# Performance work log

Measured on AMD Instinct MI355X. Metric: run time of the kernel, lower is better.

## Reference

```python
import jax, jax.numpy as jnp
import numpy as np

CLASS_EMBED_DIM = 128
TOPK = 64
EPS = float(np.finfo(float).eps)
ALPHA = 0.99


def setup_inputs() -> dict:
    key = jax.random.key(0)
    k1, k2, k3 = jax.random.split(key, 3)
    b, n, d = 16, 256, 640  # d = embed_dim + class_embed_dim
    embed_dim, inner_dim = 512, 512
    x = jax.random.normal(k1, (b, n, d), dtype=jnp.float32)
    # kaiming-normal style init: std = sqrt(2 / fan_in)
    std = (2.0 / embed_dim) ** 0.5
    Wq = jax.random.normal(k2, (embed_dim, inner_dim), dtype=jnp.float32) * std
    Wk = jax.random.normal(k3, (embed_dim, inner_dim), dtype=jnp.float32) * std
    alpha = jnp.float32(ALPHA)
    return {"x": x, "Wq": Wq, "Wk": Wk, "alpha": alpha}


def reference(x, Wq, Wk, alpha):
    b, n, d = x.shape
    xf = x.reshape(b * n, d)            # (N, embed+class)
    xe = xf[:, :-CLASS_EMBED_DIM]       # (N, embed)
    q = xe @ Wq                         # (N, inner)
    k = xe @ Wk                         # (N, inner)
    D = q.shape[1]
    # dots[i,j] = mean_d (q_i - k_j)^2, via expansion (avoids N x N x D tensor)
    q2 = jnp.sum(q * q, axis=1)
    k2 = jnp.sum(k * k, axis=1)
    dots = (q2[:, None] + k2[None, :] - 2.0 * (q @ k.T)) / D  # (N, N)
    N = dots.shape[0]
    _, idx = jax.lax.top_k(dots, TOPK)  # largest, matching torch.topk
    mask = jnp.zeros_like(dots).at[jnp.arange(N)[:, None], idx].set(1.0)
    mask = ((mask + mask.T) > 0).astype(jnp.float32)
    attn = dots * mask
    A = jnp.eye(N, dtype=dots.dtype) - alpha * attn + EPS
    out = jnp.linalg.inv(A) @ xf        # (N, d); to_v is identity
    return out.reshape(b, n, d)
```

## Files before the change

kernel.cpp:

```cpp
#include <hip/hip_runtime.h>
#include <float.h>

#define NN 4096
#define DD 640
#define DE 512
#define NB 16
#define NPAN (NN/NB)
#define SB 128
#define NSB (NN/SB)

static __device__ __forceinline__ float4 ldg4(const float* p) { return *(const float4*)p; }

__global__ __launch_bounds__(256) void proj_gemm(
    const float* __restrict__ xf, const float* __restrict__ Wq,
    const float* __restrict__ Wk, float* __restrict__ q, float* __restrict__ kk_)
{
  __shared__ float Xs[32][68], Qs[32][68], Ks[32][68];
  const int i0 = blockIdx.x * 64, c0 = blockIdx.y * 64;
  const int t = threadIdx.x, tr = t >> 4, tc = t & 15;
  float accq[4][4] = {}, acck[4][4] = {};
  for (int kb = 0; kb < DE; kb += 32) {
    {
      int m = t >> 3, k4 = (t & 7) << 2;
      float4 v0 = ldg4(xf + (size_t)(i0 + m) * DD + kb + k4);
      float4 v1 = ldg4(xf + (size_t)(i0 + m + 32) * DD + kb + k4);
      Xs[k4+0][m] = v0.x; Xs[k4+1][m] = v0.y; Xs[k4+2][m] = v0.z; Xs[k4+3][m] = v0.w;
      Xs[k4+0][m+32] = v1.x; Xs[k4+1][m+32] = v1.y; Xs[k4+2][m+32] = v1.z; Xs[k4+3][m+32] = v1.w;
    }
    {
      int kr = t >> 3, n8 = (t & 7) << 3;
      *(float4*)&Qs[kr][n8]   = ldg4(Wq + (size_t)(kb + kr) * DE + c0 + n8);
      *(float4*)&Qs[kr][n8+4] = ldg4(Wq + (size_t)(kb + kr) * DE + c0 + n8 + 4);
      *(float4*)&Ks[kr][n8]   = ldg4(Wk + (size_t)(kb + kr) * DE + c0 + n8);
      *(float4*)&Ks[kr][n8+4] = ldg4(Wk + (size_t)(kb + kr) * DE + c0 + n8 + 4);
    }
    __syncthreads();
    #pragma unroll
    for (int kkk = 0; kkk < 32; ++kkk) {
      float a[4], bq[4], bk[4];
      *(float4*)a  = *(const float4*)&Xs[kkk][tr << 2];
      *(float4*)bq = *(const float4*)&Qs[kkk][tc << 2];
      *(float4*)bk = *(const float4*)&Ks[kkk][tc << 2];
      #pragma unroll
      for (int r = 0; r < 4; ++r)
        #pragma unroll
        for (int c = 0; c < 4; ++c) { accq[r][c] += a[r]*bq[c]; acck[r][c] += a[r]*bk[c]; }
    }
    __syncthreads();
  }
  #pragma unroll
  for (int r = 0; r < 4; ++r) {
    float* qp = q   + (size_t)(i0 + (tr<<2) + r) * DE + c0 + (tc<<2);
    float* kp = kk_ + (size_t)(i0 + (tr<<2) + r) * DE + c0 + (tc<<2);
    *(float4*)qp = make_float4(accq[r][0], accq[r][1], accq[r][2], accq[r][3]);
    *(float4*)kp = make_float4(acck[r][0], acck[r][1], acck[r][2], acck[r][3]);
  }
}

__global__ __launch_bounds__(256) void rownorm(
    const float* __restrict__ q, const float* __restrict__ kk_,
    float* __restrict__ q2, float* __restrict__ k2)
{
  int w = (blockIdx.x * 256 + threadIdx.x) >> 6;
  int lane = threadIdx.x & 63;
  const float* src = (w < NN) ? q : kk_;
  int row = (w < NN) ? w : w - NN;
  const float* p = src + (size_t)row * DE;
  float s = 0.f;
  for (int c = lane; c < DE; c += 64) { float v = p[c]; s += v * v; }
  for (int off = 32; off; off >>= 1) s += __shfl_down(s, off);
  if (lane == 0) { if (w < NN) q2[row] = s; else k2[row] = s; }
}

__global__ __launch_bounds__(256) void dots_gemm(
    const float* __restrict__ q, const float* __restrict__ kk_,
    const float* __restrict__ q2, const float* __restrict__ k2,
    float* __restrict__ dots)
{
  __shared__ float Qs[32][68], Ks[32][68];
  const int i0 = blockIdx.x * 64, j0 = blockIdx.y * 64;
  const int t = threadIdx.x, tr = t >> 4, tc = t & 15;
  float acc[4][4] = {};
  for (int kb = 0; kb < DE; kb += 32) {
    int m = t >> 3, k4 = (t & 7) << 2;
    {
      float4 v0 = ldg4(q + (size_t)(i0 + m) * DE + kb + k4);
      float4 v1 = ldg4(q + (size_t)(i0 + m + 32) * DE + kb + k4);
      Qs[k4+0][m] = v0.x; Qs[k4+1][m] = v0.y; Qs[k4+2][m] = v0.z; Qs[k4+3][m] = v0.w;
      Qs[k4+0][m+32] = v1.x; Qs[k4+1][m+32] = v1.y; Qs[k4+2][m+32] = v1.z; Qs[k4+3][m+32] = v1.w;
    }
    {
      float4 v0 = ldg4(kk_ + (size_t)(j0 + m) * DE + kb + k4);
      float4 v1 = ldg4(kk_ + (size_t)(j0 + m + 32) * DE + kb + k4);
      Ks[k4+0][m] = v0.x; Ks[k4+1][m] = v0.y; Ks[k4+2][m] = v0.z; Ks[k4+3][m] = v0.w;
      Ks[k4+0][m+32] = v1.x; Ks[k4+1][m+32] = v1.y; Ks[k4+2][m+32] = v1.z; Ks[k4+3][m+32] = v1.w;
    }
    __syncthreads();
    #pragma unroll
    for (int kkk = 0; kkk < 32; ++kkk) {
      float a[4], b[4];
      *(float4*)a = *(const float4*)&Qs[kkk][tr << 2];
      *(float4*)b = *(const float4*)&Ks[kkk][tc << 2];
      #pragma unroll
      for (int r = 0; r < 4; ++r)
        #pragma unroll
        for (int c = 0; c < 4; ++c) acc[r][c] += a[r]*b[c];
    }
    __syncthreads();
  }
  const float inv = 1.0f / (float)DE;
  float k2v[4]; *(float4*)k2v = ldg4(k2 + j0 + (tc<<2));
  #pragma unroll
  for (int r = 0; r < 4; ++r) {
    float q2v = q2[i0 + (tr<<2) + r];
    float o[4];
    #pragma unroll
    for (int c = 0; c < 4; ++c) o[c] = (q2v + k2v[c] - 2.0f*acc[r][c]) * inv;
    *(float4*)(dots + (size_t)(i0 + (tr<<2) + r) * NN + j0 + (tc<<2)) =
        make_float4(o[0], o[1], o[2], o[3]);
  }
}

__global__ __launch_bounds__(256) void topk_bits(
    const float* __restrict__ dots, unsigned int* __restrict__ bits)
{
  __shared__ float row[NN];
  __shared__ unsigned int b[128];
  __shared__ float rv[4]; __shared__ int ri[4];
  const int i = blockIdx.x, t = threadIdx.x;
  const float* dr = dots + (size_t)i * NN;
  for (int c = t; c < NN; c += 256) row[c] = dr[c];
  if (t < 128) b[t] = 0u;
  __syncthreads();
  for (int it = 0; it < 64; ++it) {
    float bv = -FLT_MAX; int bi = NN;
    for (int c = t; c < NN; c += 256) { float v = row[c]; if (v > bv) { bv = v; bi = c; } }
    for (int off = 32; off; off >>= 1) {
      float ov = __shfl_down(bv, off); int oi = __shfl_down(bi, off);
      if (ov > bv || (ov == bv && oi < bi)) { bv = ov; bi = oi; }
    }
    if ((t & 63) == 0) { rv[t >> 6] = bv; ri[t >> 6] = bi; }
    __syncthreads();
    if (t == 0) {
      float fv = rv[0]; int fi = ri[0];
      for (int w = 1; w < 4; ++w)
        if (rv[w] > fv || (rv[w] == fv && ri[w] < fi)) { fv = rv[w]; fi = ri[w]; }
      b[fi >> 5] |= 1u << (fi & 31);
      row[fi] = -FLT_MAX;
    }
    __syncthreads();
  }
  if (t < 128) bits[(size_t)i * 128 + t] = b[t];
}

__global__ __launch_bounds__(256) void build_A(
    float* __restrict__ A, const unsigned int* __restrict__ bits,
    const float* __restrict__ alpha_p)
{
  int tid = blockIdx.x * 256 + threadIdx.x;
  int i = tid >> 10;
  int j4 = (tid & 1023) << 2;
  float alpha = alpha_p[0];
  float* p = A + (size_t)i * NN + j4;
  float4 d = *(float4*)p;
  unsigned int wrow = bits[(size_t)i * 128 + (j4 >> 5)];
  float dv[4] = {d.x, d.y, d.z, d.w}, o[4];
  #pragma unroll
  for (int u = 0; u < 4; ++u) {
    int j = j4 + u;
    unsigned int m1 = (wrow >> (j & 31)) & 1u;
    unsigned int m2 = (bits[(size_t)j * 128 + (i >> 5)] >> (i & 31)) & 1u;
    float base = (i == j) ? 1.0f : 0.0f;
    o[u] = base - ((m1 | m2) ? alpha * dv[u] : 0.0f);
  }
  *(float4*)p = make_float4(o[0], o[1], o[2], o[3]);
}

__global__ __launch_bounds__(1024) void lu_panel(
    float* __restrict__ A, int k0, int* __restrict__ piv,
    int* __restrict__ pr_dst, int* __restrict__ pr_src)
{
  const int t = threadIdx.x;
  const int M = NN - k0;
  float a[4][NB];
  __shared__ float bufA[NB], bufB[NB];
  __shared__ float rv[16]; __shared__ int ri[16];
  __shared__ int s_pr;
  __shared__ int piv_s[NB];

  #pragma unroll
  for (int i = 0; i < 4; ++i) {
    int r = t + (i << 10);
    if (r < M) {
      const float* src = A + (size_t)(k0 + r) * NN + k0;
      #pragma unroll
      for (int c4 = 0; c4 < NB; c4 += 4) {
        float4 v = ldg4(src + c4);
        a[i][c4] = v.x; a[i][c4+1] = v.y; a[i][c4+2] = v.z; a[i][c4+3] = v.w;
      }
    }
  }

  #pragma unroll
  for (int j = 0; j < NB; ++j) {
    float bv = -1.0f; int br = 1 << 30;
    #pragma unroll
    for (int i = 0; i < 4; ++i) {
      int r = t + (i << 10);
      if (r >= j && r < M) {
        float v = fabsf(a[i][j]);
        if (v > bv || (v == bv && r < br)) { bv = v; br = r; }
      }
    }
    for (int off = 32; off; off >>= 1) {
      float ov = __shfl_down(bv, off); int orr = __shfl_down(br, off);
      if (ov > bv || (ov == bv && orr < br)) { bv = ov; br = orr; }
    }
    if ((t & 63) == 0) { rv[t >> 6] = bv; ri[t >> 6] = br; }
    __syncthreads();
    if (t == 0) {
      float fv = rv[0]; int fr = ri[0];
      for (int w = 1; w < 16; ++w)
        if (rv[w] > fv || (rv[w] == fv && ri[w] < fr)) { fv = rv[w]; fr = ri[w]; }
      s_pr = fr; piv_s[j] = k0 + fr;
    }
    __syncthreads();
    const int pr = s_pr, prT = pr & 1023, prS = pr >> 10;
    if (t == prT) {
      #pragma unroll
      for (int i2 = 0; i2 < 4; ++i2) if (i2 == prS) {
        #pragma unroll
        for (int c = 0; c < NB; ++c) bufB[c] = a[i2][c];
      }
    }
    if (t == j) {
      #pragma unroll
      for (int c = 0; c < NB; ++c) bufA[c] = a[0][c];
    }
    __syncthreads();
    if (t == j) {
      #pragma unroll
      for (int c = 0; c < NB; ++c) a[0][c] = bufB[c];
    }
    if (t == prT) {
      #pragma unroll
      for (int i2 = 0; i2 < 4; ++i2) if (i2 == prS) {
        #pragma unroll
        for (int c = 0; c < NB; ++c) a[i2][c] = bufA[c];
      }
    }
    float rp = 1.0f / bufB[j];
    #pragma unroll
    for (int i = 0; i < 4; ++i) {
      int r = t + (i << 10);
      if (r > j && r < M) {
        float mlt = a[i][j] * rp;
        a[i][j] = mlt;
        #pragma unroll
        for (int c = j + 1; c < NB; ++c) a[i][c] -= mlt * bufB[c];
      }
    }
    __syncthreads();
  }

  #pragma unroll
  for (int i = 0; i < 4; ++i) {
    int r = t + (i << 10);
    if (r < M) {
      float* dst = A + (size_t)(k0 + r) * NN + k0;
      #pragma unroll
      for (int c4 = 0; c4 < NB; c4 += 4)
        *(float4*)(dst + c4) = make_float4(a[i][c4], a[i][c4+1], a[i][c4+2], a[i][c4+3]);
    }
  }
  if (t < NB) piv[k0 + t] = piv_s[t];

  if (t < 32) {
    int slotrow = (t < NB) ? (k0 + t) : -1;
    int content = slotrow;
    int next_ext = NB;
    for (int j = 0; j < NB; ++j) {
      int p = piv_s[j];
      unsigned long long mask = __ballot(slotrow == p);
      int bslot;
      if (mask) bslot = __ffsll((unsigned long long)mask) - 1;
      else {
        bslot = next_ext;
        if (t == next_ext) { slotrow = p; content = p; }
        next_ext++;
      }
      int srcl = (t == j) ? bslot : ((t == bslot) ? j : t);
      content = __shfl(content, srcl);
    }
    pr_dst[t] = slotrow;
    pr_src[t] = content;
  }
}

__global__ __launch_bounds__(256) void laswp_pairs(
    float* __restrict__ A, int k0,
    const int* __restrict__ pr_dst, const int* __restrict__ pr_src)
{
  __shared__ int sd[32], ss[32];
  int t = threadIdx.x;
  if (t < 32) { sd[t] = pr_dst[t]; ss[t] = pr_src[t]; }
  __syncthreads();
  int cg = blockIdx.x * 256 + t;
  if (cg >= NN - NB) return;
  int c = (cg < k0) ? cg : cg + NB;
  float tmp[32];
  #pragma unroll
  for (int i = 0; i < 32; ++i)
    tmp[i] = (sd[i] >= 0 && sd[i] != ss[i]) ? A[(size_t)ss[i] * NN + c] : 0.0f;
  #pragma unroll
  for (int i = 0; i < 32; ++i)
    if (sd[i] >= 0 && sd[i] != ss[i]) A[(size_t)sd[i] * NN + c] = tmp[i];
}

__global__ __launch_bounds__(256) void trsm16(float* __restrict__ A, int k0)
{
  __shared__ float l[16][17];
  int t = threadIdx.x;
  if (t < 256) {
    int i = t >> 4, j = t & 15;
    l[i][j] = A[(size_t)(k0 + i) * NN + k0 + j];
  }
  __syncthreads();
  int c = k0 + NB + blockIdx.x * 256 + t;
  if (c >= NN) return;
  float x[16];
  #pragma unroll
  for (int i = 0; i < 16; ++i) x[i] = A[(size_t)(k0 + i) * NN + c];
  #pragma unroll
  for (int i = 1; i < 16; ++i)
    #pragma unroll
    for (int j = 0; j < i; ++j) x[i] -= l[i][j] * x[j];
  #pragma unroll
  for (int i = 0; i < 16; ++i) A[(size_t)(k0 + i) * NN + c] = x[i];
}

__global__ __launch_bounds__(256) void rank_update(
    float* __restrict__ C, int ldc,
    const float* __restrict__ Aop, int lda,
    const float* __restrict__ Bop, int ldb,
    int Mr, int Nc, int K)
{
  __shared__ float As[16][68], Bs[16][68];
  const int m0 = blockIdx.x * 64, n0 = blockIdx.y * 64;
  const int t = threadIdx.x, tr = t >> 4, tc = t & 15;
  const float4 z4 = make_float4(0.f, 0.f, 0.f, 0.f);
  float acc[4][4] = {};
  for (int kb = 0; kb < K; kb += 16) {
    {
      int m = t >> 2, k4 = (t & 3) << 2;
      float4 v0 = (m0 + m < Mr) ? ldg4(Aop + (size_t)(m0 + m) * lda + kb + k4) : z4;
      As[k4+0][m] = v0.x; As[k4+1][m] = v0.y; As[k4+2][m] = v0.z; As[k4+3][m] = v0.w;
    }
    {
      int kr = t >> 4, n4 = (t & 15) << 2;
      bool ok = (n0 + n4 < Nc);
      float4 w0 = ok ? ldg4(Bop + (size_t)(kb + kr) * ldb + n0 + n4) : z4;
      *(float4*)&Bs[kr][n4] = w0;
    }
    __syncthreads();
    #pragma unroll
    for (int kkk = 0; kkk < 16; ++kkk) {
      float a[4], b[4];
      *(float4*)a = *(const float4*)&As[kkk][tr << 2];
      *(float4*)b = *(const float4*)&Bs[kkk][tc << 2];
      #pragma unroll
      for (int r = 0; r < 4; ++r)
        #pragma unroll
        for (int c = 0; c < 4; ++c) acc[r][c] += a[r] * b[c];
    }
    __syncthreads();
  }
  #pragma unroll
  for (int r = 0; r < 4; ++r) {
    int m = m0 + (tr << 2) + r;
    int n = n0 + (tc << 2);
    if (m < Mr && n < Nc) {
      float* cp = C + (size_t)m * ldc + n;
      float4 cv = *(float4*)cp;
      cv.x -= acc[r][0]; cv.y -= acc[r][1]; cv.z -= acc[r][2]; cv.w -= acc[r][3];
      *(float4*)cp = cv;
    }
  }
}

__global__ __launch_bounds__(128) void inv_tri(
    const float* __restrict__ Ag, float* __restrict__ invT, int upper)
{
  __shared__ float xs[128][128];
  const int s = blockIdx.x, t = threadIdx.x;
  const size_t r0 = (size_t)s * SB;
  for (int i = 0; i < 128; ++i) xs[i][t] = 0.0f;
  const float* Tb = Ag + r0 * NN + r0;
  if (!upper) {
    xs[t][t] = 1.0f;
    for (int i = 1; i < 128; ++i) {
      float ssum = 0.f;
      for (int j = 0; j < i; ++j) ssum += Tb[(size_t)i * NN + j] * xs[j][t];
      if (i != t) xs[i][t] = -ssum;
    }
  } else {
    xs[t][t] = 1.0f / Tb[(size_t)t * NN + t];
    for (int i = 126; i >= 0; --i) {
      float ssum = 0.f;
      for (int j = i + 1; j < 128; ++j) ssum += Tb[(size_t)i * NN + j] * xs[j][t];
      if (i != t) xs[i][t] = -ssum / Tb[(size_t)i * NN + i];
    }
  }
  for (int i = 0; i < 128; ++i) invT[(size_t)s * SB * SB + (size_t)i * SB + t] = xs[i][t];
}

__global__ __launch_bounds__(1024) void perm_compose(
    const int* __restrict__ piv, int* __restrict__ idxp)
{
  __shared__ int pl[NN];
  const int t = threadIdx.x;
  for (int j = t; j < NN; j += 1024) pl[j] = piv[j];
  __syncthreads();
  int pos[4] = { t, t + 1024, t + 2048, t + 3072 };
  for (int j = NN - 1; j >= 0; --j) {
    int p = pl[j];
    #pragma unroll
    for (int u = 0; u < 4; ++u) {
      int r = t + (u << 10);
      if (j <= r) {
        if (pos[u] == j) pos[u] = p;
        else if (pos[u] == p) pos[u] = j;
      }
    }
  }
  #pragma unroll
  for (int u = 0; u < 4; ++u) idxp[t + (u << 10)] = pos[u];
}

__global__ __launch_bounds__(256) void gather_rows(
    const float* __restrict__ xf, const int* __restrict__ idxp, float* __restrict__ out)
{
  const int r = blockIdx.x, t = threadIdx.x;
  const int src = idxp[r];
  const float4* s = (const float4*)(xf + (size_t)src * DD);
  float4* d = (float4*)(out + (size_t)r * DD);
  for (int c = t; c < DD / 4; c += 256) d[c] = s[c];
}

__global__ __launch_bounds__(256) void diag_apply(
    float* __restrict__ B, const float* __restrict__ Minv, int r0)
{
  __shared__ float Bs[128][68];
  const int c0 = blockIdx.x * 64, t = threadIdx.x;
  #pragma unroll
  for (int v = 0; v < 8; ++v) {
    int id = t + v * 256;
    int k = id >> 4, c4 = (id & 15) << 2;
    *(float4*)&Bs[k][c4] = ldg4(B + (size_t)(r0 + k) * DD + c0 + c4);
  }
  __syncthreads();
  const int tr = t >> 4, tc = t & 15;
  float acc[8][4] = {};
  for (int k4 = 0; k4 < 128; k4 += 4) {
    float b0[4], b1[4], b2[4], b3[4];
    *(float4*)b0 = *(const float4*)&Bs[k4+0][tc << 2];
    *(float4*)b1 = *(const float4*)&Bs[k4+1][tc << 2];
    *(float4*)b2 = *(const float4*)&Bs[k4+2][tc << 2];
    *(float4*)b3 = *(const float4*)&Bs[k4+3][tc << 2];
    #pragma unroll
    for (int rr = 0; rr < 8; ++rr) {
      float m[4]; *(float4*)m = ldg4(Minv + (size_t)(tr*8 + rr) * SB + k4);
      #pragma unroll
      for (int c = 0; c < 4; ++c)
        acc[rr][c] += m[0]*b0[c] + m[1]*b1[c] + m[2]*b2[c] + m[3]*b3[c];
    }
  }
  #pragma unroll
  for (int rr = 0; rr < 8; ++rr)
    *(float4*)(B + (size_t)(r0 + tr*8 + rr) * DD + c0 + (tc << 2)) =
        make_float4(acc[rr][0], acc[rr][1], acc[rr][2], acc[rr][3]);
}

extern "C" void kernel_launch(void* const* d_in, const int* in_sizes, int n_in,
                              void* d_out, int out_size, void* d_ws, size_t ws_size,
                              hipStream_t stream)
{
  const float* xf    = (const float*)d_in[0];
  const float* Wq    = (const float*)d_in[1];
  const float* Wk    = (const float*)d_in[2];
  const float* alpha = (const float*)d_in[3];
  float* out = (float*)d_out;
  char* ws = (char*)d_ws;

  float* Amat = (float*)(ws);
  float* q    = (float*)(ws + 67108864ull);
  float* kbuf = (float*)(ws + 75497472ull);
  float* invL = (float*)(ws + 83886080ull);
  float* invU = (float*)(ws + 85983232ull);
  unsigned int* bits = (unsigned int*)(ws + 88080384ull);
  float* q2   = (float*)(ws + 90177536ull);
  float* k2   = (float*)(ws + 90193920ull);
  int* piv    = (int*)(ws + 90210304ull);
  int* idxp   = (int*)(ws + 90226688ull);
  int* prd    = (int*)(ws + 90243072ull);
  int* prs    = (int*)(ws + 90275840ull);

  proj_gemm<<<dim3(NN/64, DE/64), 256, 0, stream>>>(xf, Wq, Wk, q, kbuf);
  rownorm<<<2 * NN / 4, 256, 0, stream>>>(q, kbuf, q2, k2);
  dots_gemm<<<dim3(NN/64, NN/64), 256, 0, stream>>>(q, kbuf, q2, k2, Amat);
  topk_bits<<<NN, 256, 0, stream>>>(Amat, bits);
  build_A<<<NN * NN / 4 / 256, 256, 0, stream>>>(Amat, bits, alpha);

  for (int p = 0; p < NPAN; ++p) {
    int k0 = p * NB;
    lu_panel<<<1, 1024, 0, stream>>>(Amat, k0, piv, prd + p * 32, prs + p * 32);
    laswp_pairs<<<(NN - NB + 255) / 256, 256, 0, stream>>>(Amat, k0, prd + p * 32, prs + p * 32);
    if (k0 + NB < NN) {
      int M2 = NN - k0 - NB;
      trsm16<<<(M2 + 255) / 256, 256, 0, stream>>>(Amat, k0);
      rank_update<<<dim3((M2 + 63) / 64, (M2 + 63) / 64), 256, 0, stream>>>(
          Amat + (size_t)(k0 + NB) * NN + (k0 + NB), NN,
          Amat + (size_t)(k0 + NB) * NN + k0, NN,
          Amat + (size_t)k0 * NN + (k0 + NB), NN,
          M2, M2, NB);
    }
  }

  inv_tri<<<NSB, 128, 0, stream>>>(Amat, invL, 0);
  inv_tri<<<NSB, 128, 0, stream>>>(Amat, invU, 1);
  perm_compose<<<1, 1024, 0, stream>>>(piv, idxp);
  gather_rows<<<NN, 256, 0, stream>>>(xf, idxp, out);

  for (int s = 0; s < NSB; ++s) {
    int r0 = s * SB;
    diag_apply<<<DD / 64, 256, 0, stream>>>(out, invL + (size_t)s * SB * SB, r0);
    if (r0 + SB < NN) {
      int M2 = NN - r0 - SB;
      rank_update<<<dim3(M2 / 64, DD / 64), 256, 0, stream>>>(
          out + (size_t)(r0 + SB) * DD, DD,
          Amat + (size_t)(r0 + SB) * NN + r0, NN,
          out + (size_t)r0 * DD, DD,
          M2, DD, SB);
    }
  }
  for (int s = NSB - 1; s >= 0; --s) {
    int r0 = s * SB;
    diag_apply<<<DD / 64, 256, 0, stream>>>(out, invU + (size_t)s * SB * SB, r0);
    if (r0 > 0) {
      rank_update<<<dim3(r0 / 64, DD / 64), 256, 0, stream>>>(
          out, DD,
          Amat + r0, NN,
          out + (size_t)r0 * DD, DD,
          r0, DD, SB);
    }
  }
}
```

Measured before the change: 38.61 ms.

## Restructure LU into two-level blocked factorization with 128-wide outer blocks

Replaces the right-looking LU with rank-16 trailing updates by a two-level scheme. Inner 16-column panels update only within a 128-column outer block. Row swaps are deferred and applied once per outer block through a composed permutation and a temporary buffer, a 128-wide triangular solve runs, and the trailing matrix gets one rank-128 update. The panel kernel now does the in-block row swap and the 16-wide triangular solve itself, which removes two launches per panel. This targets the launch overhead and the bandwidth-bound rank-16 updates over the full trailing matrix, at the cost of more complex permutation bookkeeping and a serial 128-step permutation kernel.

```diff
diff --git a/kernel.cpp b/kernel.cpp
--- a/kernel.cpp
+++ b/kernel.cpp
@@ -5,7 +5,8 @@
 #define DD 640
 #define DE 512
 #define NB 16
-#define NPAN (NN/NB)
+#define OB 128
+#define NOB (NN/OB)
 #define SB 128
 #define NSB (NN/SB)
 
@@ -177,8 +178,7 @@
 }
 
 __global__ __launch_bounds__(1024) void lu_panel(
-    float* __restrict__ A, int k0, int* __restrict__ piv,
-    int* __restrict__ pr_dst, int* __restrict__ pr_src)
+    float* __restrict__ A, int k0, int ok0, int* __restrict__ piv)
 {
   const int t = threadIdx.x;
   const int M = NN - k0;
@@ -187,6 +187,9 @@
   __shared__ float rv[16]; __shared__ int ri[16];
   __shared__ int s_pr;
   __shared__ int piv_s[NB];
+  __shared__ int sd[32], ss[32];
+  __shared__ float l16[16][17];
+  __shared__ float gbuf[32][112];
 
   #pragma unroll
   for (int i = 0; i < 4; ++i) {
@@ -274,6 +277,11 @@
     }
   }
   if (t < NB) piv[k0 + t] = piv_s[t];
+
+  if (t < 16) {
+    #pragma unroll
+    for (int c2 = 0; c2 < NB; ++c2) l16[t][c2] = a[0][c2];
+  }
 
   if (t < 32) {
     int slotrow = (t < NB) ? (k0 + t) : -1;
@@ -292,51 +300,132 @@
       int srcl = (t == j) ? bslot : ((t == bslot) ? j : t);
       content = __shfl(content, srcl);
     }
-    pr_dst[t] = slotrow;
-    pr_src[t] = content;
-  }
-}
-
-__global__ __launch_bounds__(256) void laswp_pairs(
-    float* __restrict__ A, int k0,
-    const int* __restrict__ pr_dst, const int* __restrict__ pr_src)
-{
-  __shared__ int sd[32], ss[32];
-  int t = threadIdx.x;
-  if (t < 32) { sd[t] = pr_dst[t]; ss[t] = pr_src[t]; }
-  __syncthreads();
-  int cg = blockIdx.x * 256 + t;
-  if (cg >= NN - NB) return;
-  int c = (cg < k0) ? cg : cg + NB;
-  float tmp[32];
-  #pragma unroll
-  for (int i = 0; i < 32; ++i)
-    tmp[i] = (sd[i] >= 0 && sd[i] != ss[i]) ? A[(size_t)ss[i] * NN + c] : 0.0f;
-  #pragma unroll
-  for (int i = 0; i < 32; ++i)
-    if (sd[i] >= 0 && sd[i] != ss[i]) A[(size_t)sd[i] * NN + c] = tmp[i];
-}
-
-__global__ __launch_bounds__(256) void trsm16(float* __restrict__ A, int k0)
-{
-  __shared__ float l[16][17];
-  int t = threadIdx.x;
-  if (t < 256) {
-    int i = t >> 4, j = t & 15;
-    l[i][j] = A[(size_t)(k0 + i) * NN + k0 + j];
-  }
-  __syncthreads();
-  int c = k0 + NB + blockIdx.x * 256 + t;
-  if (c >= NN) return;
-  float x[16];
-  #pragma unroll
-  for (int i = 0; i < 16; ++i) x[i] = A[(size_t)(k0 + i) * NN + c];
-  #pragma unroll
-  for (int i = 1; i < 16; ++i)
-    #pragma unroll
-    for (int j = 0; j < i; ++j) x[i] -= l[i][j] * x[j];
-  #pragma unroll
-  for (int i = 0; i < 16; ++i) A[(size_t)(k0 + i) * NN + c] = x[i];
+    sd[t] = slotrow;
+    ss[t] = content;
+  }
+  __syncthreads();
+
+  const int p16 = k0 - ok0;
+  for (int idx = t; idx < 32 * 112; idx += 1024) {
+    int i = idx / 112, cc = idx - i * 112;
+    if (sd[i] >= 0 && sd[i] != ss[i]) {
+      int c = ok0 + (cc < p16 ? cc : cc + NB);
+      gbuf[i][cc] = A[(size_t)ss[i] * NN + c];
+    }
+  }
+  __syncthreads();
+  for (int idx = t; idx < 32 * 112; idx += 1024) {
+    int i = idx / 112, cc = idx - i * 112;
+    if (sd[i] >= 0 && sd[i] != ss[i]) {
+      int c = ok0 + (cc < p16 ? cc : cc + NB);
+      A[(size_t)sd[i] * NN + c] = gbuf[i][cc];
+    }
+  }
+  __syncthreads();
+
+  const int w = ok0 + OB - (k0 + NB);
+  if (t < w) {
+    int c = k0 + NB + t;
+    int cc = p16 + t;
+    float x[16];
+    #pragma unroll
+    for (int i = 0; i < 16; ++i)
+      x[i] = (ss[i] != sd[i]) ? gbuf[i][cc] : A[(size_t)(k0 + i) * NN + c];
+    #pragma unroll
+    for (int i = 1; i < 16; ++i)
+      #pragma unroll
+      for (int j = 0; j < i; ++j) x[i] -= l16[i][j] * x[j];
+    #pragma unroll
+    for (int i = 0; i < 16; ++i) A[(size_t)(k0 + i) * NN + c] = x[i];
+  }
+}
+
+__global__ __launch_bounds__(128) void net_perm128(
+    const int* __restrict__ piv_g, int ok0,
+    int* __restrict__ nd, int* __restrict__ ns)
+{
+  __shared__ int slotrow[256], content[256];
+  __shared__ int found, next_ext;
+  const int t = threadIdx.x;
+  slotrow[t] = ok0 + t;       content[t] = ok0 + t;
+  slotrow[t + 128] = -1;      content[t + 128] = -1;
+  if (t == 0) next_ext = 128;
+  for (int j = 0; j < OB; ++j) {
+    __syncthreads();
+    int p = piv_g[ok0 + j];
+    if (t == 0) found = (p < ok0 + OB) ? (p - ok0) : -1;
+    __syncthreads();
+    if (p >= ok0 + OB && slotrow[t + 128] == p) found = t + 128;
+    __syncthreads();
+    if (t == 0) {
+      int s2 = found;
+      if (s2 < 0) { s2 = next_ext++; slotrow[s2] = p; content[s2] = p; }
+      int tmp = content[j]; content[j] = content[s2]; content[s2] = tmp;
+    }
+  }
+  __syncthreads();
+  nd[t] = slotrow[t];           ns[t] = content[t];
+  nd[t + 128] = slotrow[t + 128]; ns[t + 128] = content[t + 128];
+}
+
+__global__ __launch_bounds__(256) void perm_copy_out(
+    const float* __restrict__ A, float* __restrict__ T,
+    const int* __restrict__ nd, const int* __restrict__ ns, int ok0)
+{
+  int s = blockIdx.y;
+  int d = nd[s], sr = ns[s];
+  if (d < 0 || d == sr) return;
+  int c = blockIdx.x * 1024 + threadIdx.x * 4;
+  if (c >= ok0 && c < ok0 + OB) return;
+  *(float4*)(T + (size_t)s * NN + c) = ldg4(A + (size_t)sr * NN + c);
+}
+
+__global__ __launch_bounds__(256) void perm_copy_in(
+    float* __restrict__ A, const float* __restrict__ T,
+    const int* __restrict__ nd, const int* __restrict__ ns, int ok0)
+{
+  int s = blockIdx.y;
+  int d = nd[s], sr = ns[s];
+  if (d < 0 || d == sr) return;
+  int c = blockIdx.x * 1024 + threadIdx.x * 4;
+  if (c >= ok0 && c < ok0 + OB) return;
+  *(float4*)(A + (size_t)d * NN + c) = ldg4(T + (size_t)s * NN + c);
+}
+
+__global__ __launch_bounds__(64) void trsm128L(float* __restrict__ A, int ok0)
+{
+  __shared__ float Ls[64][65];
+  __shared__ float xs[64][132];
+  const int t = threadIdx.x;
+  const int c = ok0 + OB + blockIdx.x * 64 + t;
+  for (int i = 0; i < 128; ++i) xs[t][i] = A[(size_t)(ok0 + i) * NN + c];
+  for (int i = 0; i < 64; ++i) Ls[i][t] = A[(size_t)(ok0 + i) * NN + ok0 + t];
+  __syncthreads();
+  for (int i = 1; i < 64; ++i) {
+    float s = 0.f;
+    #pragma unroll 4
+    for (int j = 0; j < i; ++j) s += Ls[i][j] * xs[t][j];
+    xs[t][i] -= s;
+  }
+  __syncthreads();
+  for (int i = 0; i < 64; ++i) Ls[i][t] = A[(size_t)(ok0 + 64 + i) * NN + ok0 + t];
+  __syncthreads();
+  for (int i = 0; i < 64; ++i) {
+    float s = 0.f;
+    #pragma unroll 4
+    for (int j = 0; j < 64; ++j) s += Ls[i][j] * xs[t][j];
+    xs[t][64 + i] -= s;
+  }
+  __syncthreads();
+  for (int i = 0; i < 64; ++i) Ls[i][t] = A[(size_t)(ok0 + 64 + i) * NN + ok0 + 64 + t];
+  __syncthreads();
+  for (int i = 1; i < 64; ++i) {
+    float s = 0.f;
+    #pragma unroll 4
+    for (int j = 0; j < i; ++j) s += Ls[i][j] * xs[t][64 + j];
+    xs[t][64 + i] -= s;
+  }
+  for (int i = 0; i < 128; ++i) A[(size_t)(ok0 + i) * NN + c] = xs[t][i];
 }
 
 __global__ __launch_bounds__(256) void rank_update(
@@ -502,8 +591,9 @@
   float* k2   = (float*)(ws + 90193920ull);
   int* piv    = (int*)(ws + 90210304ull);
   int* idxp   = (int*)(ws + 90226688ull);
-  int* prd    = (int*)(ws + 90243072ull);
-  int* prs    = (int*)(ws + 90275840ull);
+  int* nd     = (int*)(ws + 90243072ull);
+  int* ns     = (int*)(ws + 90275840ull);
+  float* Tbuf = q;
 
   proj_gemm<<<dim3(NN/64, DE/64), 256, 0, stream>>>(xf, Wq, Wk, q, kbuf);
   rownorm<<<2 * NN / 4, 256, 0, stream>>>(q, kbuf, q2, k2);
@@ -511,18 +601,34 @@
   topk_bits<<<NN, 256, 0, stream>>>(Amat, bits);
   build_A<<<NN * NN / 4 / 256, 256, 0, stream>>>(Amat, bits, alpha);
 
-  for (int p = 0; p < NPAN; ++p) {
-    int k0 = p * NB;
-    lu_panel<<<1, 1024, 0, stream>>>(Amat, k0, piv, prd + p * 32, prs + p * 32);
-    laswp_pairs<<<(NN - NB + 255) / 256, 256, 0, stream>>>(Amat, k0, prd + p * 32, prs + p * 32);
-    if (k0 + NB < NN) {
-      int M2 = NN - k0 - NB;
-      trsm16<<<(M2 + 255) / 256, 256, 0, stream>>>(Amat, k0);
-      rank_update<<<dim3((M2 + 63) / 64, (M2 + 63) / 64), 256, 0, stream>>>(
-          Amat + (size_t)(k0 + NB) * NN + (k0 + NB), NN,
-          Amat + (size_t)(k0 + NB) * NN + k0, NN,
-          Amat + (size_t)k0 * NN + (k0 + NB), NN,
-          M2, M2, NB);
+  for (int ob = 0; ob < NOB; ++ob) {
+    const int ok0 = ob * OB;
+    for (int p = 0; p < OB / NB; ++p) {
+      const int k0 = ok0 + p * NB;
+      lu_panel<<<1, 1024, 0, stream>>>(Amat, k0, ok0, piv);
+      if (p < OB / NB - 1) {
+        const int k1 = k0 + NB;
+        const int w = ok0 + OB - k1;
+        const int M2 = NN - k1;
+        rank_update<<<dim3((M2 + 63) / 64, (w + 63) / 64), 256, 0, stream>>>(
+            Amat + (size_t)k1 * NN + k1, NN,
+            Amat + (size_t)k1 * NN + k0, NN,
+            Amat + (size_t)k0 * NN + k1, NN,
+            M2, w, NB);
+      }
+    }
+    net_perm128<<<1, 128, 0, stream>>>(piv, ok0, nd, ns);
+    perm_copy_out<<<dim3(NN / 1024, 256), 256, 0, stream>>>(Amat, Tbuf, nd, ns, ok0);
+    perm_copy_in<<<dim3(NN / 1024, 256), 256, 0, stream>>>(Amat, Tbuf, nd, ns, ok0);
+    const int b1 = ok0 + OB;
+    const int M2 = NN - b1;
+    if (M2 > 0) {
+      trsm128L<<<M2 / 64, 64, 0, stream>>>(Amat, ok0);
+      rank_update<<<dim3(M2 / 64, M2 / 64), 256, 0, stream>>>(
+          Amat + (size_t)b1 * NN + b1, NN,
+          Amat + (size_t)b1 * NN + ok0, NN,
+          Amat + (size_t)ok0 * NN + b1, NN,
+          M2, M2, OB);
     }
   }
 
```

Result: slower. 40.80 ms (+5.7%).
